# Performance work log

Measured on AMD Instinct MI355X. Metric: run time of the kernel, lower is better.

## Reference

```python
import jax, jax.numpy as jnp
import numpy as np

N = 50000       # nodes
E = 800000      # edges (before self-loops)
G = 64          # graphs in batch
F_IN = 128      # node_features
HID = 64        # hidden_channels
H1 = 8          # conv1 heads
NEG_SLOPE = 0.2
EPS = 1e-16


def _gat_layer(x, src, dst, W, att_src, att_dst, bias, heads, out_ch, concat):
    """PyG GATConv (eval mode: dropout inactive). src/dst include self-loops.
    x: [N, F_in]; W: [F_in, heads*out_ch]; att_*: [heads, out_ch]; bias: [heads*out_ch] or [out_ch]."""
    n = x.shape[0]
    h = (x @ W).reshape(n, heads, out_ch)                 # [N,H,C]
    a_s = jnp.sum(h * att_src, axis=-1)                   # [N,H]
    a_d = jnp.sum(h * att_dst, axis=-1)                   # [N,H]
    e = jax.nn.leaky_relu(a_s[src] + a_d[dst], NEG_SLOPE)  # [Etot,H]
    # segment softmax over incoming edges of each destination node
    m = jax.ops.segment_max(e, dst, num_segments=n)       # [N,H]
    e = jnp.exp(e - m[dst])
    denom = jax.ops.segment_sum(e, dst, num_segments=n)   # [N,H]
    alpha = e / (denom[dst] + EPS)                        # [Etot,H]
    msg = h[src] * alpha[:, :, None]                      # [Etot,H,C]
    out = jax.ops.segment_sum(msg, dst, num_segments=n)   # [N,H,C]
    if concat:
        out = out.reshape(n, heads * out_ch)
    else:
        out = out.mean(axis=1)
    return out + bias


def setup_inputs() -> dict:
    key = jax.random.key(0)
    ks = jax.random.split(key, 14)
    x = jax.random.normal(ks[0], (N, F_IN), dtype=jnp.float32)
    edge_index = jax.random.randint(ks[1], (2, E), 0, N, dtype=jnp.int64)
    batch_index = jnp.sort(jax.random.randint(ks[2], (N,), 0, G, dtype=jnp.int64))
    s = 0.05
    return {
        "x": x,
        "edge_index": edge_index,
        "batch_index": batch_index,
        "W1": jax.random.normal(ks[3], (F_IN, H1 * HID), dtype=jnp.float32) * s,
        "att_src1": jax.random.normal(ks[4], (H1, HID), dtype=jnp.float32) * s,
        "att_dst1": jax.random.normal(ks[5], (H1, HID), dtype=jnp.float32) * s,
        "b1": jnp.zeros((H1 * HID,), dtype=jnp.float32),
        "W2": jax.random.normal(ks[6], (H1 * HID, HID), dtype=jnp.float32) * s,
        "att_src2": jax.random.normal(ks[7], (1, HID), dtype=jnp.float32) * s,
        "att_dst2": jax.random.normal(ks[8], (1, HID), dtype=jnp.float32) * s,
        "b2": jnp.zeros((HID,), dtype=jnp.float32),
        "lin_W": jax.random.normal(ks[9], (HID, 1), dtype=jnp.float32) * s,
        "lin_b": jnp.zeros((1,), dtype=jnp.float32),
    }


def reference(x, edge_index, batch_index, W1, att_src1, att_dst1, b1,
              W2, att_src2, att_dst2, b2, lin_W, lin_b):
    n = x.shape[0]
    loops = jnp.arange(n, dtype=edge_index.dtype)
    src = jnp.concatenate([edge_index[0], loops])
    dst = jnp.concatenate([edge_index[1], loops])
    # eval mode: F.dropout is identity
    h = jax.nn.elu(_gat_layer(x, src, dst, W1, att_src1, att_dst1, b1, H1, HID, True))
    h = _gat_layer(h, src, dst, W2, att_src2, att_dst2, b2, 1, HID, False)
    # global mean pool over graphs
    sums = jax.ops.segment_sum(h, batch_index, num_segments=G)          # [G,HID]
    cnt = jax.ops.segment_sum(jnp.ones((n,), h.dtype), batch_index, num_segments=G)
    pooled = sums / jnp.maximum(cnt, 1.0)[:, None]
    return pooled @ lin_W + lin_b                                       # [G,1]
```

## Files before the change

kernel.cpp:

```cpp
#include <hip/hip_runtime.h>
#include <math.h>

#define NN 50000
#define EE 800000
#define ET 850000
#define GG 64
#define MPAD 50048
#define NCAP 64
#define NROW 50016
#define CSRI (NROW * NCAP)

typedef __attribute__((ext_vector_type(8))) short bf16x8;
typedef __attribute__((ext_vector_type(4))) float f32x4;

__device__ __forceinline__ float lrelu(float v) { return v > 0.f ? v : 0.2f * v; }

__device__ __forceinline__ unsigned short f2bf(float f) {
  unsigned u = __float_as_uint(f);
  u += 0x7FFFu + ((u >> 16) & 1u);
  return (unsigned short)(u >> 16);
}
__device__ __forceinline__ unsigned pack2(float a, float b) {
  return (unsigned)f2bf(a) | ((unsigned)f2bf(b) << 16);
}
__device__ __forceinline__ void i8acc(uint2 u, float a, float* o) {
  o[0] += a * (float)((int)(u.x << 24) >> 24);
  o[1] += a * (float)((int)(u.x << 16) >> 24);
  o[2] += a * (float)((int)(u.x <<  8) >> 24);
  o[3] += a * (float)((int)u.x >> 24);
  o[4] += a * (float)((int)(u.y << 24) >> 24);
  o[5] += a * (float)((int)(u.y << 16) >> 24);
  o[6] += a * (float)((int)(u.y <<  8) >> 24);
  o[7] += a * (float)((int)u.y >> 24);
}

#define INIT_BLOCKS 1563
#define CVT_X_BLOCKS 3128
#define CVT_W_BLOCKS 256
#define V_BLOCKS 2
#define GSEG_BLOCKS 196
__global__ __launch_bounds__(256) void prep_kernel(const float* __restrict__ x,
                                                   const float* __restrict__ W1,
                                                   const float* __restrict__ W2,
                                                   const float* __restrict__ att_s2,
                                                   const float* __restrict__ att_d2,
                                                   const float* __restrict__ linW,
                                                   const int* __restrict__ batch,
                                                   unsigned short* __restrict__ xb,
                                                   unsigned short* __restrict__ W1T,
                                                   float* __restrict__ Vs,
                                                   float* __restrict__ Vd,
                                                   float* __restrict__ Vz,
                                                   int* __restrict__ gstart,
                                                   int* __restrict__ cursor,
                                                   unsigned short* __restrict__ csr) {
  int b = blockIdx.x;
  if (b < INIT_BLOCKS) {
    int i = b * 256 + threadIdx.x;
    if (i < CSRI / 8) {
      uint4 sf = {0xC350C350u, 0xC350C350u, 0xC350C350u, 0xC350C350u};
      ((uint4*)csr)[i] = sf;
    }
    if (i < NROW) cursor[i] = 0;
  } else if (b < INIT_BLOCKS + CVT_X_BLOCKS) {
    int i8 = (b - INIT_BLOCKS) * 256 + threadIdx.x;
    if (i8 >= MPAD * 128 / 8) return;
    size_t e0 = (size_t)i8 * 8;
    int row = (int)(e0 >> 7);
    uint4 o;
    if (row < NN) {
      float4 f0 = *(const float4*)(x + e0);
      float4 f1 = *(const float4*)(x + e0 + 4);
      o.x = pack2(f0.x, f0.y); o.y = pack2(f0.z, f0.w);
      o.z = pack2(f1.x, f1.y); o.w = pack2(f1.z, f1.w);
    } else {
      o.x = o.y = o.z = o.w = 0u;
    }
    *(uint4*)(xb + e0) = o;
  } else if (b < INIT_BLOCKS + CVT_X_BLOCKS + CVT_W_BLOCKS) {
    int i = (b - INIT_BLOCKS - CVT_X_BLOCKS) * 256 + threadIdx.x;
    int k = i >> 9, n = i & 511;
    W1T[n * 128 + k] = f2bf(W1[i]);
  } else if (b < INIT_BLOCKS + CVT_X_BLOCKS + CVT_W_BLOCKS + V_BLOCKS) {
    int k = (b - INIT_BLOCKS - CVT_X_BLOCKS - CVT_W_BLOCKS) * 256 + threadIdx.x;
    float vs = 0.f, vd = 0.f, vz = 0.f;
#pragma unroll 8
    for (int c = 0; c < 64; ++c) {
      float w = W2[k * 64 + c];
      vs += w * att_s2[c];
      vd += w * att_d2[c];
      vz += w * linW[c];
    }
    Vs[k] = vs; Vd[k] = vd; Vz[k] = vz;
  } else {
    int e = (b - INIT_BLOCKS - CVT_X_BLOCKS - CVT_W_BLOCKS - V_BLOCKS) * 256 + threadIdx.x;
    if (e < NN) {
      int bb = batch[e];
      if (e == 0) {
        for (int g = 0; g <= bb; ++g) gstart[g] = 0;
      } else {
        int pb = batch[e - 1];
        for (int g = pb + 1; g <= bb; ++g) gstart[g] = e;
      }
      if (e == NN - 1) {
        for (int g = bb + 1; g <= GG; ++g) gstart[g] = NN;
      }
    }
  }
}

#define GEMM_BLOCKS 3128
#define SCAT_BLOCKS 831
#define SCAT_STRIDE (SCAT_BLOCKS * 256)
__global__ __launch_bounds__(256) void gemm1_scatter(const unsigned short* __restrict__ xb,
                                                     const unsigned short* __restrict__ W1T,
                                                     const float* __restrict__ att_s,
                                                     const float* __restrict__ att_d,
                                                     unsigned char* __restrict__ h1i,
                                                     float2* __restrict__ asc,
                                                     float* __restrict__ ad1,
                                                     const int* __restrict__ ei,
                                                     int* __restrict__ cursor,
                                                     unsigned short* __restrict__ csr) {
  __shared__ unsigned char st8[2][64 * 72];
  const int idx = blockIdx.x;
  const bool is_scat = ((idx & 3) == 3) && ((idx >> 2) < SCAT_BLOCKS);
  if (is_scat) {
    int base = (idx >> 2) * 256 + threadIdx.x;
#pragma unroll
    for (int k = 0; k < 4; ++k) {
      int e = base + k * SCAT_STRIDE;
      if (e < ET) {
        int src = (e < EE) ? ei[e] : (e - EE);
        int dst = (e < EE) ? ei[EE + e] : (e - EE);
        int pos = atomicAdd(&cursor[dst], 1);
        if (pos < NCAP) csr[(size_t)dst * NCAP + pos] = (unsigned short)src;
      }
    }
    return;
  }
  const int gi = idx - min((idx + 1) >> 2, SCAT_BLOCKS);

  const int t = threadIdx.x, w = t >> 6, l = t & 63;
  const int bm = (gi >> 2) * 64;
  const int ypair = gi & 3;
  const int m16 = l & 15, q = l >> 4;
  const int row = bm + w * 16 + m16;

  const bf16x8* Ap = (const bf16x8*)(xb + (size_t)row * 128 + q * 8);
  bf16x8 a0 = Ap[0], a1 = Ap[4], a2 = Ap[8], a3 = Ap[12];

  const int r2 = t >> 2, c16 = (t & 3) * 16;

#pragma unroll
  for (int hh = 0; hh < 2; ++hh) {
    const int h = ypair * 2 + hh;
    const bf16x8* Bp = (const bf16x8*)(W1T + (size_t)(h * 64 + m16) * 128 + q * 8);
    f32x4 acc[4] = {};
#pragma unroll
    for (int c = 0; c < 4; ++c) {
      acc[c] = __builtin_amdgcn_mfma_f32_16x16x32_bf16(a0, Bp[(size_t)c * 256 + 0],  acc[c], 0, 0, 0);
      acc[c] = __builtin_amdgcn_mfma_f32_16x16x32_bf16(a1, Bp[(size_t)c * 256 + 4],  acc[c], 0, 0, 0);
      acc[c] = __builtin_amdgcn_mfma_f32_16x16x32_bf16(a2, Bp[(size_t)c * 256 + 8],  acc[c], 0, 0, 0);
      acc[c] = __builtin_amdgcn_mfma_f32_16x16x32_bf16(a3, Bp[(size_t)c * 256 + 12], acc[c], 0, 0, 0);
    }

    float ps[4] = {0.f, 0.f, 0.f, 0.f}, pd[4] = {0.f, 0.f, 0.f, 0.f};
    float pm[4];
#pragma unroll
    for (int r = 0; r < 4; ++r)
      pm[r] = fmaxf(fmaxf(fabsf(acc[0][r]), fabsf(acc[1][r])),
                    fmaxf(fabsf(acc[2][r]), fabsf(acc[3][r])));
#pragma unroll
    for (int c = 0; c < 4; ++c) {
      float ws = att_s[h * 64 + m16 + 16 * c];
      float wd = att_d[h * 64 + m16 + 16 * c];
#pragma unroll
      for (int r = 0; r < 4; ++r) {
        ps[r] += acc[c][r] * ws;
        pd[r] += acc[c][r] * wd;
      }
    }
#pragma unroll
    for (int off = 1; off < 16; off <<= 1) {
#pragma unroll
      for (int r = 0; r < 4; ++r) {
        ps[r] += __shfl_xor(ps[r], off);
        pd[r] += __shfl_xor(pd[r], off);
        pm[r] = fmaxf(pm[r], __shfl_xor(pm[r], off));
      }
    }
    if (m16 == 0) {
#pragma unroll
      for (int r = 0; r < 4; ++r) {
        int rr = bm + w * 16 + q * 4 + r;
        float2 av;
        av.x = (rr < NN) ? ps[r] : -1e30f;
        av.y = pm[r] * (1.0f / 127.0f);
        asc[rr * 8 + h] = av;
        ad1[rr * 8 + h] = (rr < NN) ? pd[r] : 0.f;
      }
    }

    float invq[4];
#pragma unroll
    for (int r = 0; r < 4; ++r)
      invq[r] = 127.0f * __builtin_amdgcn_rcpf(fmaxf(pm[r], 1e-30f));
#pragma unroll
    for (int c = 0; c < 4; ++c)
#pragma unroll
      for (int r = 0; r < 4; ++r) {
        int qv = (int)__builtin_rintf(acc[c][r] * invq[r]);
        st8[hh][(w * 16 + q * 4 + r) * 72 + m16 + 16 * c] = (unsigned char)(qv & 0xFF);
      }
    __syncthreads();
    const unsigned* sp = (const unsigned*)(st8[hh] + r2 * 72 + c16);
    uint4 o4; o4.x = sp[0]; o4.y = sp[1]; o4.z = sp[2]; o4.w = sp[3];
    *(uint4*)(h1i + (size_t)(bm + r2) * 512 + h * 64 + c16) = o4;
  }
}

#define ISSUE8(K, U0, U1, U2, U3, U4, U5, U6, U7, ASV, SCV) do {             \
    uint4 cc;                                                                \
    cc.x = __shfl(cb.x, (K)); cc.y = __shfl(cb.y, (K));                      \
    cc.z = __shfl(cb.z, (K)); cc.w = __shfl(cb.w, (K));                      \
    unsigned pr = (slot_a & 4) ? ((slot_a & 2) ? cc.w : cc.z)                \
                               : ((slot_a & 2) ? cc.y : cc.x);               \
    int my_src = (slot_a & 1) ? (int)(pr >> 16) : (int)(pr & 0xFFFFu);       \
    float2 av = asc[my_src * 8 + ha];                                        \
    ASV = av.x; SCV = av.y;                                                  \
    int s0 = (int)(cc.x & 0xFFFFu), s1 = (int)(cc.x >> 16);                  \
    int s2 = (int)(cc.y & 0xFFFFu), s3 = (int)(cc.y >> 16);                  \
    int s4 = (int)(cc.z & 0xFFFFu), s5 = (int)(cc.z >> 16);                  \
    int s6 = (int)(cc.w & 0xFFFFu), s7 = (int)(cc.w >> 16);                  \
    U0 = *(const uint2*)(h1i + (size_t)s0 * 512 + lane * 8);                 \
    U1 = *(const uint2*)(h1i + (size_t)s1 * 512 + lane * 8);                 \
    U2 = *(const uint2*)(h1i + (size_t)s2 * 512 + lane * 8);                 \
    U3 = *(const uint2*)(h1i + (size_t)s3 * 512 + lane * 8);                 \
    U4 = *(const uint2*)(h1i + (size_t)s4 * 512 + lane * 8);                 \
    U5 = *(const uint2*)(h1i + (size_t)s5 * 512 + lane * 8);                 \
    U6 = *(const uint2*)(h1i + (size_t)s6 * 512 + lane * 8);                 \
    U7 = *(const uint2*)(h1i + (size_t)s7 * 512 + lane * 8);                 \
  } while (0)

#define PROC8(U0, U1, U2, U3, U4, U5, U6, U7, ASV, SCV) do {                 \
    float myal = __expf(lrelu((ASV) + adv_a));                               \
    float d8 = myal;                                                         \
    d8 += __shfl_xor(d8, 1); d8 += __shfl_xor(d8, 2); d8 += __shfl_xor(d8, 4);\
    den += d8;                                                               \
    float ac = myal * (SCV);                                                 \
    float a0 = __shfl(ac, hb + 0), a1 = __shfl(ac, hb + 1);                  \
    float a2 = __shfl(ac, hb + 2), a3 = __shfl(ac, hb + 3);                  \
    float a4 = __shfl(ac, hb + 4), a5 = __shfl(ac, hb + 5);                  \
    float a6 = __shfl(ac, hb + 6), a7 = __shfl(ac, hb + 7);                  \
    i8acc(U0, a0, o); i8acc(U1, a1, o);                                      \
    i8acc(U2, a2, o); i8acc(U3, a3, o);                                      \
    i8acc(U4, a4, o); i8acc(U5, a5, o);                                      \
    i8acc(U6, a6, o); i8acc(U7, a7, o);                                      \
  } while (0)

__global__ __launch_bounds__(256) void agg1_kernel(const unsigned char* __restrict__ h1i,
                                                   const float2* __restrict__ asc,
                                                   const float* __restrict__ ad1,
                                                   const int* __restrict__ cnt,
                                                   const unsigned short* __restrict__ csr,
                                                   const float* __restrict__ b1,
                                                   const float* __restrict__ Vs,
                                                   const float* __restrict__ Vd,
                                                   const float* __restrict__ Vz,
                                                   float2* __restrict__ azz,
                                                   float* __restrict__ ad2) {
  int dst = blockIdx.x * 4 + (threadIdx.x >> 6);
  int lane = threadIdx.x & 63;
  if (dst >= NN) return;
  const int ha = lane >> 3;
  const int hb = ha * 8;
  const int slot_a = lane & 7;

  const int cv = min(cnt[dst], NCAP);
  const uint4 cb = *(const uint4*)(csr + (size_t)dst * NCAP + (lane & 7) * 8);
  const float adv_a = ad1[dst * 8 + ha];
  const int nb = (cv + 7) >> 3;

  float den = 0.f;
  float o[8] = {0.f, 0.f, 0.f, 0.f, 0.f, 0.f, 0.f, 0.f};
  uint2 A0, A1, A2, A3, A4, A5, A6, A7;
  uint2 B0, B1, B2, B3, B4, B5, B6, B7;
  uint2 C0, C1, C2, C3, C4, C5, C6, C7;
  float asA, asB, asC, scA, scB, scC;

  ISSUE8(0, A0, A1, A2, A3, A4, A5, A6, A7, asA, scA);
  if (nb > 1) ISSUE8(1, B0, B1, B2, B3, B4, B5, B6, B7, asB, scB);
  int k = 0;
  for (;;) {
    if (k + 2 < nb) ISSUE8(k + 2, C0, C1, C2, C3, C4, C5, C6, C7, asC, scC);
    PROC8(A0, A1, A2, A3, A4, A5, A6, A7, asA, scA);
    if (++k >= nb) break;
    if (k + 2 < nb) ISSUE8(k + 2, A0, A1, A2, A3, A4, A5, A6, A7, asA, scA);
    PROC8(B0, B1, B2, B3, B4, B5, B6, B7, asB, scB);
    if (++k >= nb) break;
    if (k + 2 < nb) ISSUE8(k + 2, B0, B1, B2, B3, B4, B5, B6, B7, asB, scB);
    PROC8(C0, C1, C2, C3, C4, C5, C6, C7, asC, scC);
    if (++k >= nb) break;
  }
  float inv = 1.0f / (den + 1e-16f);

  const float4* bp = (const float4*)(b1 + lane * 8);
  float4 bb0 = bp[0], bb1 = bp[1];
  float bb[8] = {bb0.x, bb0.y, bb0.z, bb0.w, bb1.x, bb1.y, bb1.z, bb1.w};
  float v[8];
#pragma unroll
  for (int j = 0; j < 8; ++j) {
    float t = o[j] * inv + bb[j];
    v[j] = (t > 0.f) ? t : (__expf(t) - 1.0f);
  }

  const float4* vsp = (const float4*)(Vs + lane * 8);
  const float4* vdp = (const float4*)(Vd + lane * 8);
  const float4* vzp = (const float4*)(Vz + lane * 8);
  float4 vs0 = vsp[0], vs1 = vsp[1];
  float4 vd0 = vdp[0], vd1 = vdp[1];
  float4 vz0 = vzp[0], vz1 = vzp[1];
  float ps = v[0]*vs0.x + v[1]*vs0.y + v[2]*vs0.z + v[3]*vs0.w
           + v[4]*vs1.x + v[5]*vs1.y + v[6]*vs1.z + v[7]*vs1.w;
  float pd = v[0]*vd0.x + v[1]*vd0.y + v[2]*vd0.z + v[3]*vd0.w
           + v[4]*vd1.x + v[5]*vd1.y + v[6]*vd1.z + v[7]*vd1.w;
  float pz = v[0]*vz0.x + v[1]*vz0.y + v[2]*vz0.z + v[3]*vz0.w
           + v[4]*vz1.x + v[5]*vz1.y + v[6]*vz1.z + v[7]*vz1.w;
#pragma unroll
  for (int off = 1; off < 64; off <<= 1) {
    ps += __shfl_xor(ps, off);
    pd += __shfl_xor(pd, off);
    pz += __shfl_xor(pz, off);
  }
  if (lane == 0) {
    float2 az; az.x = ps; az.y = pz;
    azz[dst] = az;
    ad2[dst] = pd;
  }
}

__global__ __launch_bounds__(256) void agg2z_kernel(const float2* __restrict__ azz,
                                                    const float* __restrict__ ad2,
                                                    const int* __restrict__ cnt,
                                                    const unsigned short* __restrict__ csr,
                                                    float* __restrict__ s) {
  int dst = blockIdx.x * 4 + (threadIdx.x >> 6);
  int lane = threadIdx.x & 63;
  if (dst >= NN) return;
  const int si = dst * NCAP, e = si + min(cnt[dst], NCAP);
  const float adv = ad2[dst];
  float num = 0.f, den = 0.f;
  for (int i = si + lane; i < e; i += 64) {
    int src = csr[i];
    float2 az = azz[src];
    float a = __expf(lrelu(az.x + adv));
    num += a * az.y;
    den += a;
  }
#pragma unroll
  for (int off = 32; off > 0; off >>= 1) {
    num += __shfl_xor(num, off);
    den += __shfl_xor(den, off);
  }
  if (lane == 0) s[dst] = num / (den + 1e-16f);
}

__global__ __launch_bounds__(256) void poolz_kernel(const float* __restrict__ s,
                                                    const int* __restrict__ gstart,
                                                    const float* __restrict__ b2,
                                                    const float* __restrict__ linW,
                                                    const float* __restrict__ linb,
                                                    float* __restrict__ out) {
  __shared__ float red[4];
  int g = blockIdx.x;
  int t = threadIdx.x, lane = t & 63, w = t >> 6;
  int s0 = gstart[g], e0 = gstart[g + 1];
  float acc = 0.f;
  for (int i = s0 + t; i < e0; i += 256) acc += s[i];
#pragma unroll
  for (int off = 32; off > 0; off >>= 1) acc += __shfl_xor(acc, off);
  if (lane == 0) red[w] = acc;
  __syncthreads();
  if (w == 0) {
    float total = red[0] + red[1] + red[2] + red[3];
    float bz = b2[lane] * linW[lane];
#pragma unroll
    for (int off = 32; off > 0; off >>= 1) bz += __shfl_xor(bz, off);
    if (lane == 0) {
      float cnt = fmaxf((float)(e0 - s0), 1.0f);
      out[g] = total / cnt + bz + linb[0];
    }
  }
}

extern "C" void kernel_launch(void* const* d_in, const int* in_sizes, int n_in,
                              void* d_out, int out_size, void* d_ws, size_t ws_size,
                              hipStream_t stream) {
  const float* x      = (const float*)d_in[0];
  const int*   ei     = (const int*)d_in[1];
  const int*   batch  = (const int*)d_in[2];
  const float* W1     = (const float*)d_in[3];
  const float* att_s1 = (const float*)d_in[4];
  const float* att_d1 = (const float*)d_in[5];
  const float* b1     = (const float*)d_in[6];
  const float* W2     = (const float*)d_in[7];
  const float* att_s2 = (const float*)d_in[8];
  const float* att_d2 = (const float*)d_in[9];
  const float* b2     = (const float*)d_in[10];
  const float* linW   = (const float*)d_in[11];
  const float* linb   = (const float*)d_in[12];
  float* out = (float*)d_out;

  char* base = (char*)d_ws;
  unsigned short* xb  = (unsigned short*)base; base += (size_t)MPAD * 128 * 2;
  unsigned char*  h1i = (unsigned char*)base;  base += (size_t)MPAD * 512;
  unsigned short* W1T = (unsigned short*)base; base += (size_t)512 * 128 * 2;
  float* Vs   = (float*)base; base += (size_t)512 * 4;
  float* Vd   = (float*)base; base += (size_t)512 * 4;
  float* Vz   = (float*)base; base += (size_t)512 * 4;
  float2* asc = (float2*)base; base += (size_t)MPAD * 8 * 8;
  float* ad1  = (float*)base; base += (size_t)MPAD * 8 * 4;
  float2* azz = (float2*)base; base += (size_t)NROW * 8;
  float* ad2  = (float*)base; base += (size_t)NROW * 4;
  float* sv   = (float*)base; base += (size_t)NROW * 4;
  int* cursor = (int*)base;  base += (size_t)NROW * 4;
  unsigned short* csr = (unsigned short*)base; base += (size_t)CSRI * 2;
  int* gstart = (int*)base;  base += (size_t)(GG + 16) * 4;

  if (ws_size < (size_t)(base - (char*)d_ws)) return;

  prep_kernel<<<INIT_BLOCKS + CVT_X_BLOCKS + CVT_W_BLOCKS + V_BLOCKS + GSEG_BLOCKS,
                256, 0, stream>>>(x, W1, W2, att_s2, att_d2, linW, batch,
                                  xb, W1T, Vs, Vd, Vz, gstart, cursor, csr);

  gemm1_scatter<<<GEMM_BLOCKS + SCAT_BLOCKS, 256, 0, stream>>>(
      xb, W1T, att_s1, att_d1, h1i, asc, ad1, ei, cursor, csr);

  agg1_kernel<<<12500, 256, 0, stream>>>(h1i, asc, ad1, cursor, csr, b1,
                                         Vs, Vd, Vz, azz, ad2);

  agg2z_kernel<<<12500, 256, 0, stream>>>(azz, ad2, cursor, csr, sv);
  poolz_kernel<<<GG, 256, 0, stream>>>(sv, gstart, b2, linW, linb, out);
}
```

Measured before the change: 284.5 us.

## Build CSR via shared-memory binned scan then compact, replacing global atomics

The per-edge global atomicAdd scatter into a padded CSR is replaced by two stages. In the first, 512 blocks each own a destination range and an edge chunk and bin sources with LDS atomics into a per-chunk sub-CSR. In the second, overlapped with the GEMM, each destination row is compacted with warp shuffles, the self-loop is placed first and the tail is padded to a multiple of 8 with the sentinel. This removes the large CSR fill and the contended global atomics, but each scan block now reads an entire 100K-edge destination chunk, which multiplies reads of the edge list. The agg1 prefetch pipeline is also cut from three buffers to two, presumably to ease register pressure.

```diff
diff --git a/kernel.cpp b/kernel.cpp
--- a/kernel.cpp
+++ b/kernel.cpp
@@ -3,12 +3,12 @@
 
 #define NN 50000
 #define EE 800000
-#define ET 850000
 #define GG 64
 #define MPAD 50048
 #define NCAP 64
 #define NROW 50016
 #define CSRI (NROW * NCAP)
+#define NDST 50048
 
 typedef __attribute__((ext_vector_type(8))) short bf16x8;
 typedef __attribute__((ext_vector_type(4))) float f32x4;
@@ -34,7 +34,8 @@
   o[7] += a * (float)((int)u.y >> 24);
 }
 
-#define INIT_BLOCKS 1563
+#define SCAN_B 512
+#define DR2 782
 #define CVT_X_BLOCKS 3128
 #define CVT_W_BLOCKS 256
 #define V_BLOCKS 2
@@ -46,24 +47,51 @@
                                                    const float* __restrict__ att_d2,
                                                    const float* __restrict__ linW,
                                                    const int* __restrict__ batch,
+                                                   const int* __restrict__ ei,
                                                    unsigned short* __restrict__ xb,
                                                    unsigned short* __restrict__ W1T,
                                                    float* __restrict__ Vs,
                                                    float* __restrict__ Vd,
                                                    float* __restrict__ Vz,
                                                    int* __restrict__ gstart,
-                                                   int* __restrict__ cursor,
-                                                   unsigned short* __restrict__ csr) {
+                                                   int* __restrict__ cnt2,
+                                                   unsigned short* __restrict__ csr2) {
   int b = blockIdx.x;
-  if (b < INIT_BLOCKS) {
-    int i = b * 256 + threadIdx.x;
-    if (i < CSRI / 8) {
-      uint4 sf = {0xC350C350u, 0xC350C350u, 0xC350C350u, 0xC350C350u};
-      ((uint4*)csr)[i] = sf;
-    }
-    if (i < NROW) cursor[i] = 0;
-  } else if (b < INIT_BLOCKS + CVT_X_BLOCKS) {
-    int i8 = (b - INIT_BLOCKS) * 256 + threadIdx.x;
+  if (b < SCAN_B) {
+    __shared__ int lcur[DR2];
+    const int r = b >> 3, c = b & 7;
+    const int lo = r * DR2;
+    for (int j = threadIdx.x; j < DR2; j += 256) lcur[j] = 0;
+    __syncthreads();
+    const uint4* d4 = (const uint4*)(ei + EE + c * 100000);
+    const int* srcp = ei + c * 100000;
+    for (int it = 0; it < 98; ++it) {
+      int i4 = it * 256 + threadIdx.x;
+      if (i4 < 25000) {
+        uint4 dv = d4[i4];
+        int e0 = i4 * 4;
+        int dd[4] = {(int)dv.x, (int)dv.y, (int)dv.z, (int)dv.w};
+#pragma unroll
+        for (int j = 0; j < 4; ++j) {
+          unsigned rel = (unsigned)dd[j] - (unsigned)lo;
+          if (rel < (unsigned)DR2) {
+            int pos = atomicAdd(&lcur[rel], 1);
+            if (pos < 32)
+              csr2[(size_t)dd[j] * 256 + c * 32 + pos] = (unsigned short)srcp[e0 + j];
+          }
+        }
+      }
+    }
+    __syncthreads();
+    for (int j = threadIdx.x; j < DR2; j += 256) {
+      int d = lo + j;
+      if (d < NN) cnt2[d * 8 + c] = min(lcur[j], 32);
+    }
+    return;
+  }
+  int cix = b - SCAN_B;
+  if (cix < CVT_X_BLOCKS) {
+    int i8 = cix * 256 + threadIdx.x;
     if (i8 >= MPAD * 128 / 8) return;
     size_t e0 = (size_t)i8 * 8;
     int row = (int)(e0 >> 7);
@@ -77,23 +105,23 @@
       o.x = o.y = o.z = o.w = 0u;
     }
     *(uint4*)(xb + e0) = o;
-  } else if (b < INIT_BLOCKS + CVT_X_BLOCKS + CVT_W_BLOCKS) {
-    int i = (b - INIT_BLOCKS - CVT_X_BLOCKS) * 256 + threadIdx.x;
+  } else if (cix < CVT_X_BLOCKS + CVT_W_BLOCKS) {
+    int i = (cix - CVT_X_BLOCKS) * 256 + threadIdx.x;
     int k = i >> 9, n = i & 511;
     W1T[n * 128 + k] = f2bf(W1[i]);
-  } else if (b < INIT_BLOCKS + CVT_X_BLOCKS + CVT_W_BLOCKS + V_BLOCKS) {
-    int k = (b - INIT_BLOCKS - CVT_X_BLOCKS - CVT_W_BLOCKS) * 256 + threadIdx.x;
+  } else if (cix < CVT_X_BLOCKS + CVT_W_BLOCKS + V_BLOCKS) {
+    int k = (cix - CVT_X_BLOCKS - CVT_W_BLOCKS) * 256 + threadIdx.x;
     float vs = 0.f, vd = 0.f, vz = 0.f;
 #pragma unroll 8
-    for (int c = 0; c < 64; ++c) {
-      float w = W2[k * 64 + c];
-      vs += w * att_s2[c];
-      vd += w * att_d2[c];
-      vz += w * linW[c];
+    for (int cc = 0; cc < 64; ++cc) {
+      float w = W2[k * 64 + cc];
+      vs += w * att_s2[cc];
+      vd += w * att_d2[cc];
+      vz += w * linW[cc];
     }
     Vs[k] = vs; Vd[k] = vd; Vz[k] = vz;
   } else {
-    int e = (b - INIT_BLOCKS - CVT_X_BLOCKS - CVT_W_BLOCKS - V_BLOCKS) * 256 + threadIdx.x;
+    int e = (cix - CVT_X_BLOCKS - CVT_W_BLOCKS - V_BLOCKS) * 256 + threadIdx.x;
     if (e < NN) {
       int bb = batch[e];
       if (e == 0) {
@@ -110,36 +138,61 @@
 }
 
 #define GEMM_BLOCKS 3128
-#define SCAT_BLOCKS 831
-#define SCAT_STRIDE (SCAT_BLOCKS * 256)
-__global__ __launch_bounds__(256) void gemm1_scatter(const unsigned short* __restrict__ xb,
+#define CMP_BLOCKS 782
+__global__ __launch_bounds__(256) void gemm1_compact(const unsigned short* __restrict__ xb,
                                                      const unsigned short* __restrict__ W1T,
                                                      const float* __restrict__ att_s,
                                                      const float* __restrict__ att_d,
                                                      unsigned char* __restrict__ h1i,
                                                      float2* __restrict__ asc,
                                                      float* __restrict__ ad1,
-                                                     const int* __restrict__ ei,
-                                                     int* __restrict__ cursor,
+                                                     const int* __restrict__ cnt2,
+                                                     const unsigned short* __restrict__ csr2,
+                                                     int* __restrict__ cnt,
                                                      unsigned short* __restrict__ csr) {
   __shared__ unsigned char st8[2][64 * 72];
   const int idx = blockIdx.x;
-  const bool is_scat = ((idx & 3) == 3) && ((idx >> 2) < SCAT_BLOCKS);
-  if (is_scat) {
-    int base = (idx >> 2) * 256 + threadIdx.x;
-#pragma unroll
-    for (int k = 0; k < 4; ++k) {
-      int e = base + k * SCAT_STRIDE;
-      if (e < ET) {
-        int src = (e < EE) ? ei[e] : (e - EE);
-        int dst = (e < EE) ? ei[EE + e] : (e - EE);
-        int pos = atomicAdd(&cursor[dst], 1);
-        if (pos < NCAP) csr[(size_t)dst * NCAP + pos] = (unsigned short)src;
-      }
+  const bool is_cmp = ((idx & 3) == 3) && ((idx >> 2) < CMP_BLOCKS);
+  if (is_cmp) {
+    const int cb = idx >> 2;
+    const int wv = threadIdx.x >> 6, lane = threadIdx.x & 63;
+    const int myc = (lane >> 2) & 7;
+#pragma unroll 1
+    for (int di = 0; di < 16; ++di) {
+      int dst = (cb << 6) + (wv << 4) + di;
+      if (dst >= NN) continue;
+      int v = (lane < 8) ? cnt2[dst * 8 + lane] : 0;
+      int off = 1, run = 1;
+#pragma unroll
+      for (int c = 0; c < 8; ++c) {
+        int cc = __shfl(v, c);
+        if (c < myc) off += cc;
+        run += cc;
+      }
+      int mycnt = __shfl(v, myc);
+      unsigned short* orow = csr + (size_t)dst * NCAP;
+      if (lane < 32) {
+        uint4 sl = *(const uint4*)(csr2 + (size_t)dst * 256 + lane * 8);
+        unsigned short ss[8];
+        ss[0] = sl.x & 0xFFFF; ss[1] = sl.x >> 16;
+        ss[2] = sl.y & 0xFFFF; ss[3] = sl.y >> 16;
+        ss[4] = sl.z & 0xFFFF; ss[5] = sl.z >> 16;
+        ss[6] = sl.w & 0xFFFF; ss[7] = sl.w >> 16;
+        int sbase = (lane & 3) * 8;
+#pragma unroll
+        for (int j = 0; j < 8; ++j) {
+          int s = sbase + j, wi = off + s;
+          if (s < mycnt && wi < NCAP) orow[wi] = ss[j];
+        }
+      }
+      int runc = min(run, NCAP);
+      if (lane == 0) { orow[0] = (unsigned short)dst; cnt[dst] = runc; }
+      int r8 = (runc + 7) & ~7;
+      if (lane < 7 && runc + lane < r8) orow[runc + lane] = 50000;
     }
     return;
   }
-  const int gi = idx - min((idx + 1) >> 2, SCAT_BLOCKS);
+  const int gi = idx - min((idx + 1) >> 2, CMP_BLOCKS);
 
   const int t = threadIdx.x, w = t >> 6, l = t & 63;
   const int bm = (gi >> 2) * 64;
@@ -286,21 +339,16 @@
   float o[8] = {0.f, 0.f, 0.f, 0.f, 0.f, 0.f, 0.f, 0.f};
   uint2 A0, A1, A2, A3, A4, A5, A6, A7;
   uint2 B0, B1, B2, B3, B4, B5, B6, B7;
-  uint2 C0, C1, C2, C3, C4, C5, C6, C7;
-  float asA, asB, asC, scA, scB, scC;
+  float asA, asB, scA, scB;
 
   ISSUE8(0, A0, A1, A2, A3, A4, A5, A6, A7, asA, scA);
-  if (nb > 1) ISSUE8(1, B0, B1, B2, B3, B4, B5, B6, B7, asB, scB);
   int k = 0;
   for (;;) {
-    if (k + 2 < nb) ISSUE8(k + 2, C0, C1, C2, C3, C4, C5, C6, C7, asC, scC);
+    if (k + 1 < nb) ISSUE8(k + 1, B0, B1, B2, B3, B4, B5, B6, B7, asB, scB);
     PROC8(A0, A1, A2, A3, A4, A5, A6, A7, asA, scA);
     if (++k >= nb) break;
-    if (k + 2 < nb) ISSUE8(k + 2, A0, A1, A2, A3, A4, A5, A6, A7, asA, scA);
+    if (k + 1 < nb) ISSUE8(k + 1, A0, A1, A2, A3, A4, A5, A6, A7, asA, scA);
     PROC8(B0, B1, B2, B3, B4, B5, B6, B7, asB, scB);
-    if (++k >= nb) break;
-    if (k + 2 < nb) ISSUE8(k + 2, B0, B1, B2, B3, B4, B5, B6, B7, asB, scB);
-    PROC8(C0, C1, C2, C3, C4, C5, C6, C7, asC, scC);
     if (++k >= nb) break;
   }
   float inv = 1.0f / (den + 1e-16f);
@@ -421,25 +469,27 @@
   float* Vz   = (float*)base; base += (size_t)512 * 4;
   float2* asc = (float2*)base; base += (size_t)MPAD * 8 * 8;
   float* ad1  = (float*)base; base += (size_t)MPAD * 8 * 4;
-  float2* azz = (float2*)base; base += (size_t)NROW * 8;
-  float* ad2  = (float*)base; base += (size_t)NROW * 4;
-  float* sv   = (float*)base; base += (size_t)NROW * 4;
-  int* cursor = (int*)base;  base += (size_t)NROW * 4;
-  unsigned short* csr = (unsigned short*)base; base += (size_t)CSRI * 2;
+  float2* azz = (float2*)base; base += (size_t)NDST * 8;
+  float* ad2  = (float*)base; base += (size_t)NDST * 4;
+  float* sv   = (float*)base; base += (size_t)NDST * 4;
+  int* cnt    = (int*)base;  base += (size_t)NDST * 4;
+  int* cnt2   = (int*)base;  base += (size_t)NDST * 8 * 4;
+  unsigned short* csr  = (unsigned short*)base; base += (size_t)CSRI * 2;
+  unsigned short* csr2 = (unsigned short*)base; base += (size_t)NDST * 256 * 2;
   int* gstart = (int*)base;  base += (size_t)(GG + 16) * 4;
 
   if (ws_size < (size_t)(base - (char*)d_ws)) return;
 
-  prep_kernel<<<INIT_BLOCKS + CVT_X_BLOCKS + CVT_W_BLOCKS + V_BLOCKS + GSEG_BLOCKS,
-                256, 0, stream>>>(x, W1, W2, att_s2, att_d2, linW, batch,
-                                  xb, W1T, Vs, Vd, Vz, gstart, cursor, csr);
-
-  gemm1_scatter<<<GEMM_BLOCKS + SCAT_BLOCKS, 256, 0, stream>>>(
-      xb, W1T, att_s1, att_d1, h1i, asc, ad1, ei, cursor, csr);
-
-  agg1_kernel<<<12500, 256, 0, stream>>>(h1i, asc, ad1, cursor, csr, b1,
+  prep_kernel<<<SCAN_B + CVT_X_BLOCKS + CVT_W_BLOCKS + V_BLOCKS + GSEG_BLOCKS,
+                256, 0, stream>>>(x, W1, W2, att_s2, att_d2, linW, batch, ei,
+                                  xb, W1T, Vs, Vd, Vz, gstart, cnt2, csr2);
+
+  gemm1_compact<<<GEMM_BLOCKS + CMP_BLOCKS, 256, 0, stream>>>(
+      xb, W1T, att_s1, att_d1, h1i, asc, ad1, cnt2, csr2, cnt, csr);
+
+  agg1_kernel<<<12500, 256, 0, stream>>>(h1i, asc, ad1, cnt, csr, b1,
                                          Vs, Vd, Vz, azz, ad2);
 
-  agg2z_kernel<<<12500, 256, 0, stream>>>(azz, ad2, cursor, csr, sv);
+  agg2z_kernel<<<12500, 256, 0, stream>>>(azz, ad2, cnt, csr, sv);
   poolz_kernel<<<GG, 256, 0, stream>>>(sv, gstart, b2, linW, linb, out);
 }
```

Result: slower. 340.3 us (+19.6%).

## Split edge scatter across prep and GEMM kernels, drop CSR fill, shorten prefetch

Applied to the files above, without the earlier changes.

Stops pre-filling the CSR buffer with a sentinel and instead masks unused slots in the aggregation gather so they point at the padding row. The cursor is zeroed with a memset, and half of the edge scatter now runs inside the prep kernel, interleaved with the conversion blocks. The other half stays inside the GEMM kernel at a lower interleave ratio. The aggregation loop's software prefetch goes from triple to double buffering, which lowers register pressure but exposes more gather latency.

```diff
diff --git a/kernel.cpp b/kernel.cpp
--- a/kernel.cpp
+++ b/kernel.cpp
@@ -4,6 +4,7 @@
 #define NN 50000
 #define EE 800000
 #define ET 850000
+#define HALF 425000
 #define GG 64
 #define MPAD 50048
 #define NCAP 64
@@ -34,7 +35,8 @@
   o[7] += a * (float)((int)u.y >> 24);
 }
 
-#define INIT_BLOCKS 1563
+#define SCAT_P 416
+#define P_STRIDE (SCAT_P * 256)
 #define CVT_X_BLOCKS 3128
 #define CVT_W_BLOCKS 256
 #define V_BLOCKS 2
@@ -46,6 +48,7 @@
                                                    const float* __restrict__ att_d2,
                                                    const float* __restrict__ linW,
                                                    const int* __restrict__ batch,
+                                                   const int* __restrict__ ei,
                                                    unsigned short* __restrict__ xb,
                                                    unsigned short* __restrict__ W1T,
                                                    float* __restrict__ Vs,
@@ -54,16 +57,25 @@
                                                    int* __restrict__ gstart,
                                                    int* __restrict__ cursor,
                                                    unsigned short* __restrict__ csr) {
-  int b = blockIdx.x;
-  if (b < INIT_BLOCKS) {
-    int i = b * 256 + threadIdx.x;
-    if (i < CSRI / 8) {
-      uint4 sf = {0xC350C350u, 0xC350C350u, 0xC350C350u, 0xC350C350u};
-      ((uint4*)csr)[i] = sf;
-    }
-    if (i < NROW) cursor[i] = 0;
-  } else if (b < INIT_BLOCKS + CVT_X_BLOCKS) {
-    int i8 = (b - INIT_BLOCKS) * 256 + threadIdx.x;
+  const int idx = blockIdx.x;
+  const bool is_scat = ((idx & 7) == 7) && ((idx >> 3) < SCAT_P);
+  if (is_scat) {
+    int base = (idx >> 3) * 256 + threadIdx.x;
+#pragma unroll
+    for (int k = 0; k < 4; ++k) {
+      int e = base + k * P_STRIDE;
+      if (e < HALF) {
+        int src = ei[e];
+        int dst = ei[EE + e];
+        int pos = atomicAdd(&cursor[dst], 1);
+        if (pos < NCAP) csr[(size_t)dst * NCAP + pos] = (unsigned short)src;
+      }
+    }
+    return;
+  }
+  int cix = idx - min((idx + 1) >> 3, SCAT_P);
+  if (cix < CVT_X_BLOCKS) {
+    int i8 = cix * 256 + threadIdx.x;
     if (i8 >= MPAD * 128 / 8) return;
     size_t e0 = (size_t)i8 * 8;
     int row = (int)(e0 >> 7);
@@ -77,12 +89,12 @@
       o.x = o.y = o.z = o.w = 0u;
     }
     *(uint4*)(xb + e0) = o;
-  } else if (b < INIT_BLOCKS + CVT_X_BLOCKS + CVT_W_BLOCKS) {
-    int i = (b - INIT_BLOCKS - CVT_X_BLOCKS) * 256 + threadIdx.x;
+  } else if (cix < CVT_X_BLOCKS + CVT_W_BLOCKS) {
+    int i = (cix - CVT_X_BLOCKS) * 256 + threadIdx.x;
     int k = i >> 9, n = i & 511;
     W1T[n * 128 + k] = f2bf(W1[i]);
-  } else if (b < INIT_BLOCKS + CVT_X_BLOCKS + CVT_W_BLOCKS + V_BLOCKS) {
-    int k = (b - INIT_BLOCKS - CVT_X_BLOCKS - CVT_W_BLOCKS) * 256 + threadIdx.x;
+  } else if (cix < CVT_X_BLOCKS + CVT_W_BLOCKS + V_BLOCKS) {
+    int k = (cix - CVT_X_BLOCKS - CVT_W_BLOCKS) * 256 + threadIdx.x;
     float vs = 0.f, vd = 0.f, vz = 0.f;
 #pragma unroll 8
     for (int c = 0; c < 64; ++c) {
@@ -93,7 +105,7 @@
     }
     Vs[k] = vs; Vd[k] = vd; Vz[k] = vz;
   } else {
-    int e = (b - INIT_BLOCKS - CVT_X_BLOCKS - CVT_W_BLOCKS - V_BLOCKS) * 256 + threadIdx.x;
+    int e = (cix - CVT_X_BLOCKS - CVT_W_BLOCKS - V_BLOCKS) * 256 + threadIdx.x;
     if (e < NN) {
       int bb = batch[e];
       if (e == 0) {
@@ -110,8 +122,8 @@
 }
 
 #define GEMM_BLOCKS 3128
-#define SCAT_BLOCKS 831
-#define SCAT_STRIDE (SCAT_BLOCKS * 256)
+#define SCAT_G 416
+#define G_STRIDE (SCAT_G * 256)
 __global__ __launch_bounds__(256) void gemm1_scatter(const unsigned short* __restrict__ xb,
                                                      const unsigned short* __restrict__ W1T,
                                                      const float* __restrict__ att_s,
@@ -124,12 +136,12 @@
                                                      unsigned short* __restrict__ csr) {
   __shared__ unsigned char st8[2][64 * 72];
   const int idx = blockIdx.x;
-  const bool is_scat = ((idx & 3) == 3) && ((idx >> 2) < SCAT_BLOCKS);
+  const bool is_scat = ((idx & 7) == 7) && ((idx >> 3) < SCAT_G);
   if (is_scat) {
-    int base = (idx >> 2) * 256 + threadIdx.x;
+    int base = (idx >> 3) * 256 + threadIdx.x;
 #pragma unroll
     for (int k = 0; k < 4; ++k) {
-      int e = base + k * SCAT_STRIDE;
+      int e = HALF + base + k * G_STRIDE;
       if (e < ET) {
         int src = (e < EE) ? ei[e] : (e - EE);
         int dst = (e < EE) ? ei[EE + e] : (e - EE);
@@ -139,7 +151,7 @@
     }
     return;
   }
-  const int gi = idx - min((idx + 1) >> 2, SCAT_BLOCKS);
+  const int gi = idx - min((idx + 1) >> 3, SCAT_G);
 
   const int t = threadIdx.x, w = t >> 6, l = t & 63;
   const int bm = (gi >> 2) * 64;
@@ -224,15 +236,21 @@
     uint4 cc;                                                                \
     cc.x = __shfl(cb.x, (K)); cc.y = __shfl(cb.y, (K));                      \
     cc.z = __shfl(cb.z, (K)); cc.w = __shfl(cb.w, (K));                      \
+    const int lim = cv - (K) * 8;                                            \
     unsigned pr = (slot_a & 4) ? ((slot_a & 2) ? cc.w : cc.z)                \
                                : ((slot_a & 2) ? cc.y : cc.x);               \
     int my_src = (slot_a & 1) ? (int)(pr >> 16) : (int)(pr & 0xFFFFu);       \
+    my_src = (slot_a < lim) ? my_src : 50000;                                \
     float2 av = asc[my_src * 8 + ha];                                        \
     ASV = av.x; SCV = av.y;                                                  \
-    int s0 = (int)(cc.x & 0xFFFFu), s1 = (int)(cc.x >> 16);                  \
-    int s2 = (int)(cc.y & 0xFFFFu), s3 = (int)(cc.y >> 16);                  \
-    int s4 = (int)(cc.z & 0xFFFFu), s5 = (int)(cc.z >> 16);                  \
-    int s6 = (int)(cc.w & 0xFFFFu), s7 = (int)(cc.w >> 16);                  \
+    int s0 = (0 < lim) ? (int)(cc.x & 0xFFFFu) : 50000;                      \
+    int s1 = (1 < lim) ? (int)(cc.x >> 16)     : 50000;                      \
+    int s2 = (2 < lim) ? (int)(cc.y & 0xFFFFu) : 50000;                      \
+    int s3 = (3 < lim) ? (int)(cc.y >> 16)     : 50000;                      \
+    int s4 = (4 < lim) ? (int)(cc.z & 0xFFFFu) : 50000;                      \
+    int s5 = (5 < lim) ? (int)(cc.z >> 16)     : 50000;                      \
+    int s6 = (6 < lim) ? (int)(cc.w & 0xFFFFu) : 50000;                      \
+    int s7 = (7 < lim) ? (int)(cc.w >> 16)     : 50000;                      \
     U0 = *(const uint2*)(h1i + (size_t)s0 * 512 + lane * 8);                 \
     U1 = *(const uint2*)(h1i + (size_t)s1 * 512 + lane * 8);                 \
     U2 = *(const uint2*)(h1i + (size_t)s2 * 512 + lane * 8);                 \
@@ -286,21 +304,16 @@
   float o[8] = {0.f, 0.f, 0.f, 0.f, 0.f, 0.f, 0.f, 0.f};
   uint2 A0, A1, A2, A3, A4, A5, A6, A7;
   uint2 B0, B1, B2, B3, B4, B5, B6, B7;
-  uint2 C0, C1, C2, C3, C4, C5, C6, C7;
-  float asA, asB, asC, scA, scB, scC;
+  float asA, asB, scA, scB;
 
   ISSUE8(0, A0, A1, A2, A3, A4, A5, A6, A7, asA, scA);
-  if (nb > 1) ISSUE8(1, B0, B1, B2, B3, B4, B5, B6, B7, asB, scB);
   int k = 0;
   for (;;) {
-    if (k + 2 < nb) ISSUE8(k + 2, C0, C1, C2, C3, C4, C5, C6, C7, asC, scC);
+    if (k + 1 < nb) ISSUE8(k + 1, B0, B1, B2, B3, B4, B5, B6, B7, asB, scB);
     PROC8(A0, A1, A2, A3, A4, A5, A6, A7, asA, scA);
     if (++k >= nb) break;
-    if (k + 2 < nb) ISSUE8(k + 2, A0, A1, A2, A3, A4, A5, A6, A7, asA, scA);
+    if (k + 1 < nb) ISSUE8(k + 1, A0, A1, A2, A3, A4, A5, A6, A7, asA, scA);
     PROC8(B0, B1, B2, B3, B4, B5, B6, B7, asB, scB);
-    if (++k >= nb) break;
-    if (k + 2 < nb) ISSUE8(k + 2, B0, B1, B2, B3, B4, B5, B6, B7, asB, scB);
-    PROC8(C0, C1, C2, C3, C4, C5, C6, C7, asC, scC);
     if (++k >= nb) break;
   }
   float inv = 1.0f / (den + 1e-16f);
@@ -430,11 +443,14 @@
 
   if (ws_size < (size_t)(base - (char*)d_ws)) return;
 
-  prep_kernel<<<INIT_BLOCKS + CVT_X_BLOCKS + CVT_W_BLOCKS + V_BLOCKS + GSEG_BLOCKS,
-                256, 0, stream>>>(x, W1, W2, att_s2, att_d2, linW, batch,
-                                  xb, W1T, Vs, Vd, Vz, gstart, cursor, csr);
-
-  gemm1_scatter<<<GEMM_BLOCKS + SCAT_BLOCKS, 256, 0, stream>>>(
+  hipMemsetAsync(cursor, 0, (size_t)NROW * 4, stream);
+
+  prep_kernel<<<SCAT_P * 8 + (CVT_X_BLOCKS + CVT_W_BLOCKS + V_BLOCKS + GSEG_BLOCKS
+                              - SCAT_P * 8) + SCAT_P, 256, 0, stream>>>(
+      x, W1, W2, att_s2, att_d2, linW, batch, ei,
+      xb, W1T, Vs, Vd, Vz, gstart, cursor, csr);
+
+  gemm1_scatter<<<GEMM_BLOCKS + SCAT_G, 256, 0, stream>>>(
       xb, W1T, att_s1, att_d1, h1i, asc, ad1, ei, cursor, csr);
 
   agg1_kernel<<<12500, 256, 0, stream>>>(h1i, asc, ad1, cursor, csr, b1,
```

Measured after the change: 302.1 us. 1.06x slower.
